# Performance work log

Hardware: AMD Instinct MI355X
Metric: run time of the kernel (lower is better)

## Reference

```python
import jax, jax.numpy as jnp
import numpy as np
import math

N = 100000
E = 800000
H = 256
TDIM = 32
NTYPES = 22
NLAYERS = 2


def layer_norm(x, g, b, eps=1e-5):
    mu = jnp.mean(x, axis=-1, keepdims=True)
    var = jnp.var(x, axis=-1, keepdims=True)
    return (x - mu) * jax.lax.rsqrt(var + eps) * g + b


def setup_inputs() -> dict:
    key = jax.random.key(0)
    ks = jax.random.split(key, 16)
    s = 1.0 / math.sqrt(H)
    inp = {
        "clause_reprs": jax.random.normal(ks[0], (N, H), dtype=jnp.float32),
        "timestamps": jax.random.uniform(ks[1], (N,), dtype=jnp.float32) * 10000.0,
        "deriv_types": jax.random.randint(ks[2], (N,), 0, NTYPES),
        "derivation_edges": jax.random.randint(ks[3], (2, E), 0, N),
        # params
        "emb_table": jax.random.normal(ks[4], (NTYPES, H), dtype=jnp.float32),
        "temp_W": jax.random.normal(ks[5], (TDIM, H), dtype=jnp.float32) / math.sqrt(TDIM),
        "temp_b": jnp.zeros((H,), jnp.float32),
        "fus_W1": jax.random.normal(ks[6], (3 * H, H), dtype=jnp.float32) / math.sqrt(3 * H),
        "fus_b1": jnp.zeros((H,), jnp.float32),
        "fus_W2": jax.random.normal(ks[7], (H, H), dtype=jnp.float32) * s,
        "fus_b2": jnp.zeros((H,), jnp.float32),
        "in_g": jnp.ones((H,), jnp.float32),
        "in_b": jnp.zeros((H,), jnp.float32),
        "deriv_W": jax.random.normal(ks[8], (NLAYERS, 2 * H, H), dtype=jnp.float32) / math.sqrt(2 * H),
        "deriv_b": jnp.zeros((NLAYERS, H), jnp.float32),
        "dn_g": jnp.ones((NLAYERS, H), jnp.float32),
        "dn_b": jnp.zeros((NLAYERS, H), jnp.float32),
    }
    return inp


def reference(clause_reprs, timestamps, deriv_types, derivation_edges,
              emb_table, temp_W, temp_b, fus_W1, fus_b1, fus_W2, fus_b2,
              in_g, in_b, deriv_W, deriv_b, dn_g, dn_b):
    # --- temporal sinusoidal encoding -> projection ---
    half = TDIM // 2
    freqs = jnp.exp(-math.log(10000.0) * jnp.arange(half, dtype=jnp.float32) / half)
    angles = timestamps[:, None] * freqs[None, :]                      # (N, half)
    pe = jnp.concatenate([jnp.sin(angles), jnp.cos(angles)], axis=-1)  # (N, TDIM)
    temporal_enc = pe @ temp_W + temp_b                                # (N, H)
    # --- derivation type embedding ---
    deriv_enc = emb_table[deriv_types]                                 # (N, H)
    # --- input fusion + residual + LN ---
    cat = jnp.concatenate([clause_reprs, temporal_enc, deriv_enc], axis=-1)
    fused = jax.nn.relu(cat @ fus_W1 + fus_b1) @ fus_W2 + fus_b2
    x = layer_norm(fused + clause_reprs, in_g, in_b)
    # --- derivation message passing along DAG edges (parent -> child) ---
    src, dst = derivation_edges[0], derivation_edges[1]
    count = jnp.zeros((N, 1), jnp.float32).at[dst].add(1.0)
    count = jnp.maximum(count, 1.0)
    for l in range(NLAYERS):
        parent_msgs = x[src]                                           # (E, H) gather
        agg = jnp.zeros_like(x).at[dst].add(parent_msgs) / count       # (N, H) scatter-add
        combined = jnp.concatenate([x, agg], axis=-1)                  # (N, 2H)
        update = jax.nn.relu(combined @ deriv_W[l] + deriv_b[l])
        x = layer_norm(x + update, dn_g[l], dn_b[l])
    return x
```

## Files before the change

### kernel.cpp

```cpp
#include <hip/hip_runtime.h>
#include <hip/hip_bf16.h>
#include <math.h>

#define N_NODES 100000
#define N_EDGES 800000
#define H 256
#define NTYPES 22
#define SCAN_G 98
#define GRID_G ((N_NODES + 63) / 64)

typedef __attribute__((ext_vector_type(8))) short short8;
typedef __attribute__((ext_vector_type(4))) float f32x4;
typedef unsigned short u16;

__device__ __forceinline__ u16 f2bf(float f) {
    unsigned u = __float_as_uint(f);
    u += 0x7FFF + ((u >> 16) & 1);
    return (u16)(u >> 16);
}
__device__ __forceinline__ float bf2f(u16 u) {
    return __uint_as_float(((unsigned)u) << 16);
}

__device__ __forceinline__ void gload16(const void* g, void* l) {
    __builtin_amdgcn_global_load_lds(
        (const __attribute__((address_space(1))) unsigned int*)g,
        (__attribute__((address_space(3))) unsigned int*)l, 16, 0, 0);
}

__global__ __launch_bounds__(256) void prep_small(
    const float* __restrict__ temp_W, const float* __restrict__ temp_b,
    const float* __restrict__ emb, const float* __restrict__ fus_W1,
    const float* __restrict__ fus_b1,
    float* __restrict__ C1, float* __restrict__ C2, float* __restrict__ beff)
{
    int b = blockIdx.x;
    int j = threadIdx.x;
    if (b < 32) {
        float acc = 0.f;
        #pragma unroll 8
        for (int m = 0; m < H; ++m)
            acc += temp_W[b * H + m] * fus_W1[(size_t)(H + m) * H + j];
        C1[b * H + j] = acc;
    } else if (b < 32 + NTYPES) {
        int e = b - 32;
        float acc = 0.f;
        #pragma unroll 8
        for (int m = 0; m < H; ++m)
            acc += emb[e * H + m] * fus_W1[(size_t)(2 * H + m) * H + j];
        C2[e * H + j] = acc;
    } else {
        float acc = fus_b1[j];
        #pragma unroll 8
        for (int m = 0; m < H; ++m)
            acc += temp_b[m] * fus_W1[(size_t)(H + m) * H + j];
        beff[j] = acc;
    }
}

__global__ __launch_bounds__(256) void prep_frag(
    const float* __restrict__ fus_W1, const float* __restrict__ C1,
    const float* __restrict__ fus_W2, const float* __restrict__ deriv_W,
    u16* __restrict__ wblob)
{
    int s = blockIdx.x;
    const float* src; int kbase;
    if (s < 8)       { src = fus_W1;              kbase = s * 32; }
    else if (s == 8) { src = C1;                  kbase = 0; }
    else if (s < 17) { src = fus_W2;              kbase = (s - 9) * 32; }
    else if (s < 33) { src = deriv_W;             kbase = (s - 17) * 32; }
    else             { src = deriv_W + 512 * H;   kbase = (s - 33) * 32; }
    #pragma unroll
    for (int it = 0; it < 4; ++it) {
        int c = it * 256 + threadIdx.x;
        int l = c & 63, nt = c >> 6;
        int n = (nt << 4) | (l & 15);
        int k0 = kbase + ((l >> 4) << 3);
        short8 v;
        #pragma unroll
        for (int i = 0; i < 8; ++i)
            v[i] = (short)f2bf(src[(size_t)(k0 + i) * H + n]);
        *reinterpret_cast<short8*>(wblob + (size_t)s * 8192 + (size_t)c * 8) = v;
    }
}

__global__ void count_kernel(const int* __restrict__ dst, int* __restrict__ cnt)
{
    int e = blockIdx.x * blockDim.x + threadIdx.x;
    if (e < N_EDGES) atomicAdd(&cnt[dst[e]], 1);
}

__global__ __launch_bounds__(1024) void scan1_kernel(
    const int* __restrict__ cnt, int* __restrict__ off, int* __restrict__ bsum)
{
    __shared__ int s[1024];
    int i = blockIdx.x * 1024 + threadIdx.x;
    int v = (i < N_NODES) ? cnt[i] : 0;
    s[threadIdx.x] = v;
    __syncthreads();
    #pragma unroll
    for (int o = 1; o < 1024; o <<= 1) {
        int t = (threadIdx.x >= o) ? s[threadIdx.x - o] : 0;
        __syncthreads();
        s[threadIdx.x] += t;
        __syncthreads();
    }
    if (i < N_NODES) off[i] = s[threadIdx.x];
    if (threadIdx.x == 1023) bsum[blockIdx.x] = s[1023];
}

__global__ void scan2_kernel(const int* __restrict__ bsum, int* __restrict__ bbase)
{
    if (threadIdx.x == 0) {
        int acc = 0;
        for (int b = 0; b < SCAN_G; ++b) { bbase[b] = acc; acc += bsum[b]; }
    }
}

__global__ __launch_bounds__(1024) void scan3_kernel(
    int* __restrict__ off, const int* __restrict__ bbase,
    const int* __restrict__ cnt, int* __restrict__ cursor)
{
    int i = blockIdx.x * 1024 + threadIdx.x;
    if (i < N_NODES) {
        int incl = off[i] + bbase[blockIdx.x];
        off[i] = incl;
        cursor[i] = incl - cnt[i];
    }
}

__global__ void fill_kernel(const int* __restrict__ src, const int* __restrict__ dst,
                            int* __restrict__ cursor, int* __restrict__ csr)
{
    int e = blockIdx.x * blockDim.x + threadIdx.x;
    if (e < N_EDGES) {
        int pos = atomicAdd(&cursor[dst[e]], 1);
        csr[pos] = src[e];
    }
}

__global__ __launch_bounds__(256) void gather_kernel(
    const u16* __restrict__ xb, const int* __restrict__ csr,
    const int* __restrict__ off, const int* __restrict__ cnt,
    u16* __restrict__ agg)
{
    int node = blockIdx.x * 4 + (threadIdx.x >> 6);
    int l = threadIdx.x & 63;
    int deg = cnt[node];
    int start = off[node] - deg;
    float a0 = 0.f, a1 = 0.f, a2 = 0.f, a3 = 0.f;
    float b0 = 0.f, b1 = 0.f, b2 = 0.f, b3 = 0.f;
    int j = 0;
    for (; j + 1 < deg; j += 2) {
        int s0 = csr[start + j], s1 = csr[start + j + 1];
        ushort4 v0 = *reinterpret_cast<const ushort4*>(xb + (size_t)s0 * H + l * 4);
        ushort4 v1 = *reinterpret_cast<const ushort4*>(xb + (size_t)s1 * H + l * 4);
        a0 += bf2f(v0.x); a1 += bf2f(v0.y); a2 += bf2f(v0.z); a3 += bf2f(v0.w);
        b0 += bf2f(v1.x); b1 += bf2f(v1.y); b2 += bf2f(v1.z); b3 += bf2f(v1.w);
    }
    if (j < deg) {
        int s0 = csr[start + j];
        ushort4 v0 = *reinterpret_cast<const ushort4*>(xb + (size_t)s0 * H + l * 4);
        a0 += bf2f(v0.x); a1 += bf2f(v0.y); a2 += bf2f(v0.z); a3 += bf2f(v0.w);
    }
    float sc = 1.0f / fmaxf((float)deg, 1.0f);
    ushort4 o;
    o.x = f2bf((a0 + b0) * sc); o.y = f2bf((a1 + b1) * sc);
    o.z = f2bf((a2 + b2) * sc); o.w = f2bf((a3 + b3) * sc);
    *reinterpret_cast<ushort4*>(agg + (size_t)node * H + l * 4) = o;
}

__device__ __forceinline__ void mfma_step(const u16* Af, const u16* Bf,
                                          int w, int l, f32x4 acc[4][4])
{
    short8 a[4];
    #pragma unroll
    for (int m = 0; m < 4; ++m)
        a[m] = *reinterpret_cast<const short8*>(Af + (size_t)((m << 6) | l) * 8);
    #pragma unroll
    for (int n = 0; n < 4; ++n) {
        short8 b = *reinterpret_cast<const short8*>(
            Bf + (size_t)((((w << 2) | n) << 6) | l) * 8);
        #pragma unroll
        for (int m = 0; m < 4; ++m)
            acc[m][n] = __builtin_amdgcn_mfma_f32_16x16x32_bf16(a[m], b, acc[m][n],
                                                                0, 0, 0);
    }
}

__global__ __launch_bounds__(256, 3) void k12_mfma(
    const float* __restrict__ clause, const float* __restrict__ ts,
    const int* __restrict__ types, const u16* __restrict__ wblob,
    const float* __restrict__ C2, const float* __restrict__ beff,
    const float* __restrict__ b2, const float* __restrict__ gW,
    const float* __restrict__ bW, u16* __restrict__ xb)
{
    __shared__ __align__(16) u16 Af[2048];
    __shared__ __align__(16) u16 Bf[8192];
    __shared__ __align__(16) u16 hs[16384];
    int tid = threadIdx.x, w = tid >> 6, l = tid & 63;
    int g = l >> 4, c0 = l & 15;
    int i0 = blockIdx.x * 64;
    int rowA = min(i0 + ((w << 4) | c0), N_NODES - 1);
    int kcol = g << 3;
    f32x4 acc[4][4] = {};

    for (int t = 0; t < 9; ++t) {
        if (t < 8) {
            const float* p = clause + (size_t)rowA * H + t * 32 + kcol;
            float4 a = *reinterpret_cast<const float4*>(p);
            float4 b = *reinterpret_cast<const float4*>(p + 4);
            short8 v;
            v[0] = (short)f2bf(a.x); v[1] = (short)f2bf(a.y);
            v[2] = (short)f2bf(a.z); v[3] = (short)f2bf(a.w);
            v[4] = (short)f2bf(b.x); v[5] = (short)f2bf(b.y);
            v[6] = (short)f2bf(b.z); v[7] = (short)f2bf(b.w);
            *reinterpret_cast<short8*>(Af + (size_t)((w << 6) | l) * 8) = v;
        } else {
            float tsv = ts[rowA];
            short8 v;
            #pragma unroll
            for (int i = 0; i < 8; ++i) {
                int k = kcol + i;
                float fr = expf(-0.57564627324851f * (float)(k & 15));
                float ang = tsv * fr;
                float pv = (k < 16) ? sinf(ang) : cosf(ang);
                v[i] = (short)f2bf(pv);
            }
            *reinterpret_cast<short8*>(Af + (size_t)((w << 6) | l) * 8) = v;
        }
        #pragma unroll
        for (int it = 0; it < 4; ++it) {
            int c = (it << 8) + tid;
            gload16(wblob + (size_t)t * 8192 + (size_t)c * 8, Bf + (size_t)c * 8);
        }
        __syncthreads();
        mfma_step(Af, Bf, w, l, acc);
        __syncthreads();
    }

    {
        float bev[4];
        #pragma unroll
        for (int n = 0; n < 4; ++n) bev[n] = beff[(w << 6) | (n << 4) | c0];
        #pragma unroll
        for (int m = 0; m < 4; ++m) {
            #pragma unroll
            for (int r = 0; r < 4; ++r) {
                int rl = (m << 4) + (g << 2) + r;
                int tp = types[min(i0 + rl, N_NODES - 1)];
                const float* c2r = C2 + (size_t)tp * H;
                #pragma unroll
                for (int n = 0; n < 4; ++n) {
                    int col = (w << 6) | (n << 4) | c0;
                    float val = fmaxf(acc[m][n][r] + bev[n] + c2r[col], 0.f);
                    hs[((rl << 8) + col) ^ ((rl & 7) << 3)] = f2bf(val);
                }
            }
        }
    }
    __syncthreads();

    #pragma unroll
    for (int m = 0; m < 4; ++m)
        #pragma unroll
        for (int n = 0; n < 4; ++n)
            acc[m][n] = (f32x4){0.f, 0.f, 0.f, 0.f};

    for (int t = 0; t < 8; ++t) {
        #pragma unroll
        for (int it = 0; it < 4; ++it) {
            int c = (it << 8) + tid;
            gload16(wblob + (size_t)(9 + t) * 8192 + (size_t)c * 8,
                    Bf + (size_t)c * 8);
        }
        __syncthreads();
        short8 a[4];
        int colb = (t << 5) + kcol;
        #pragma unroll
        for (int m = 0; m < 4; ++m) {
            int rl2 = (m << 4) | c0;
            a[m] = *reinterpret_cast<const short8*>(
                &hs[((rl2 << 8) + colb) ^ ((c0 & 7) << 3)]);
        }
        #pragma unroll
        for (int n = 0; n < 4; ++n) {
            short8 b = *reinterpret_cast<const short8*>(
                Bf + (size_t)((((w << 2) | n) << 6) | l) * 8);
            #pragma unroll
            for (int m = 0; m < 4; ++m)
                acc[m][n] = __builtin_amdgcn_mfma_f32_16x16x32_bf16(a[m], b,
                                                                    acc[m][n], 0, 0, 0);
        }
        __syncthreads();
    }

    float2* red = reinterpret_cast<float2*>(Af);
    float bv[4], gv[4], bbv[4];
    #pragma unroll
    for (int n = 0; n < 4; ++n) {
        int col = (w << 6) | (n << 4) | c0;
        bv[n] = b2[col]; gv[n] = gW[col]; bbv[n] = bW[col];
    }
    #pragma unroll
    for (int m = 0; m < 4; ++m) {
        #pragma unroll
        for (int r = 0; r < 4; ++r) {
            int rl = (m << 4) + (g << 2) + r;
            int rowc = min(i0 + rl, N_NODES - 1);
            const float* cr = clause + (size_t)rowc * H;
            float s = 0.f, q = 0.f;
            #pragma unroll
            for (int n = 0; n < 4; ++n) {
                float pv = acc[m][n][r] + bv[n] + cr[(w << 6) | (n << 4) | c0];
                acc[m][n][r] = pv;
                s += pv; q += pv * pv;
            }
            #pragma unroll
            for (int o = 1; o < 16; o <<= 1) {
                s += __shfl_xor(s, o);
                q += __shfl_xor(q, o);
            }
            if (c0 == 0) red[(rl << 2) | w] = make_float2(s, q);
        }
    }
    __syncthreads();
    #pragma unroll
    for (int m = 0; m < 4; ++m) {
        #pragma unroll
        for (int r = 0; r < 4; ++r) {
            int rl = (m << 4) + (g << 2) + r;
            int row = i0 + rl;
            float2 t0 = red[(rl << 2) | 0], t1 = red[(rl << 2) | 1];
            float2 t2 = red[(rl << 2) | 2], t3 = red[(rl << 2) | 3];
            float S = t0.x + t1.x + t2.x + t3.x;
            float Q = t0.y + t1.y + t2.y + t3.y;
            float mu = S * (1.0f / 256.0f);
            float rstd = rsqrtf(Q * (1.0f / 256.0f) - mu * mu + 1e-5f);
            if (row < N_NODES) {
                #pragma unroll
                for (int n = 0; n < 4; ++n) {
                    int col = (w << 6) | (n << 4) | c0;
                    float val = (acc[m][n][r] - mu) * rstd * gv[n] + bbv[n];
                    xb[(size_t)row * H + col] = f2bf(val);
                }
            }
        }
    }
}

template<bool FINAL>
__global__ __launch_bounds__(256, 4) void k5_mfma(
    const u16* __restrict__ xb, const u16* __restrict__ aggb,
    const u16* __restrict__ wblob, const float* __restrict__ bl,
    const float* __restrict__ gl, const float* __restrict__ bnl,
    u16* __restrict__ xbout, float* __restrict__ xout)
{
    __shared__ __align__(16) u16 Af[4096];
    __shared__ __align__(16) u16 Bf[16384];
    int tid = threadIdx.x, w = tid >> 6, l = tid & 63;
    int g = l >> 4, c0 = l & 15;
    int i0 = blockIdx.x * 64;
    int rowA = min(i0 + ((w << 4) | c0), N_NODES - 1);
    int kcol = g << 3;
    f32x4 acc[4][4] = {};

    for (int t = 0; t < 8; ++t) {
        const u16* sb = (t < 4) ? xb : aggb;
        const u16* ap = sb + (size_t)rowA * H + ((t & 3) << 6) + kcol;
        gload16(ap,      Af + (size_t)((w << 6) | l) * 8);
        gload16(ap + 32, Af + 2048 + (size_t)((w << 6) | l) * 8);
        const u16* wk = wblob + (size_t)(t << 1) * 8192;
        #pragma unroll
        for (int it = 0; it < 4; ++it) {
            int c = (it << 8) + tid;
            gload16(wk + (size_t)c * 8,        Bf + (size_t)c * 8);
            gload16(wk + 8192 + (size_t)c * 8, Bf + 8192 + (size_t)c * 8);
        }
        __syncthreads();
        mfma_step(Af, Bf, w, l, acc);
        mfma_step(Af + 2048, Bf + 8192, w, l, acc);
        __syncthreads();
    }

    float2* red = reinterpret_cast<float2*>(Af);
    float bv[4], gv[4], bbv[4];
    #pragma unroll
    for (int n = 0; n < 4; ++n) {
        int col = (w << 6) | (n << 4) | c0;
        bv[n] = bl[col]; gv[n] = gl[col]; bbv[n] = bnl[col];
    }
    #pragma unroll
    for (int m = 0; m < 4; ++m) {
        #pragma unroll
        for (int r = 0; r < 4; ++r) {
            int rl = (m << 4) + (g << 2) + r;
            int rowc = min(i0 + rl, N_NODES - 1);
            const u16* xr = xb + (size_t)rowc * H;
            float s = 0.f, q = 0.f;
            #pragma unroll
            for (int n = 0; n < 4; ++n) {
                int col = (w << 6) | (n << 4) | c0;
                float pv = bf2f(xr[col]) + fmaxf(acc[m][n][r] + bv[n], 0.f);
                acc[m][n][r] = pv;
                s += pv; q += pv * pv;
            }
            #pragma unroll
            for (int o = 1; o < 16; o <<= 1) {
                s += __shfl_xor(s, o);
                q += __shfl_xor(q, o);
            }
            if (c0 == 0) red[(rl << 2) | w] = make_float2(s, q);
        }
    }
    __syncthreads();
    #pragma unroll
    for (int m = 0; m < 4; ++m) {
        #pragma unroll
        for (int r = 0; r < 4; ++r) {
            int rl = (m << 4) + (g << 2) + r;
            int row = i0 + rl;
            float2 t0 = red[(rl << 2) | 0], t1 = red[(rl << 2) | 1];
            float2 t2 = red[(rl << 2) | 2], t3 = red[(rl << 2) | 3];
            float S = t0.x + t1.x + t2.x + t3.x;
            float Q = t0.y + t1.y + t2.y + t3.y;
            float mu = S * (1.0f / 256.0f);
            float rstd = rsqrtf(Q * (1.0f / 256.0f) - mu * mu + 1e-5f);
            if (row < N_NODES) {
                #pragma unroll
                for (int n = 0; n < 4; ++n) {
                    int col = (w << 6) | (n << 4) | c0;
                    float val = (acc[m][n][r] - mu) * rstd * gv[n] + bbv[n];
                    if (FINAL) xout[(size_t)row * H + col] = val;
                    else       xbout[(size_t)row * H + col] = f2bf(val);
                }
            }
        }
    }
}

extern "C" void kernel_launch(void* const* d_in, const int* in_sizes, int n_in,
                              void* d_out, int out_size, void* d_ws, size_t ws_size,
                              hipStream_t stream)
{
    const float* clause  = (const float*)d_in[0];
    const float* ts      = (const float*)d_in[1];
    const int*   types   = (const int*)  d_in[2];
    const int*   edges   = (const int*)  d_in[3];
    const float* emb     = (const float*)d_in[4];
    const float* temp_W  = (const float*)d_in[5];
    const float* temp_b  = (const float*)d_in[6];
    const float* fus_W1  = (const float*)d_in[7];
    const float* fus_b1  = (const float*)d_in[8];
    const float* fus_W2  = (const float*)d_in[9];
    const float* fus_b2  = (const float*)d_in[10];
    const float* in_g    = (const float*)d_in[11];
    const float* in_b    = (const float*)d_in[12];
    const float* deriv_W = (const float*)d_in[13];
    const float* deriv_b = (const float*)d_in[14];
    const float* dn_g    = (const float*)d_in[15];
    const float* dn_b    = (const float*)d_in[16];

    char* p = (char*)d_ws;
    float* C1   = (float*)p;            p += 32 * H * 4;
    float* C2   = (float*)p;            p += NTYPES * H * 4;
    float* beff = (float*)p;            p += H * 4;
    int* cnt    = (int*)p;              p += N_NODES * 4;
    int* off    = (int*)p;              p += N_NODES * 4;
    int* cursor = (int*)p;              p += N_NODES * 4;
    int* bsum   = (int*)p;              p += 128 * 4;
    int* bbase  = (int*)p;              p += 128 * 4;
    int* csr    = (int*)p;              p += N_EDGES * 4;
    u16* wblob  = (u16*)p;              p += 49 * 8192 * 2;
    u16* xb16   = (u16*)p;              p += (size_t)N_NODES * H * 2;
    u16* aggb16 = (u16*)p;              p += (size_t)N_NODES * H * 2;
    float* x    = (float*)d_out;

    const int* src = edges;
    const int* dst = edges + N_EDGES;

    prep_small<<<32 + NTYPES + 1, 256, 0, stream>>>(temp_W, temp_b, emb, fus_W1,
                                                    fus_b1, C1, C2, beff);
    prep_frag<<<49, 256, 0, stream>>>(fus_W1, C1, fus_W2, deriv_W, wblob);

    hipMemsetAsync(cnt, 0, N_NODES * sizeof(int), stream);
    count_kernel<<<(N_EDGES + 255) / 256, 256, 0, stream>>>(dst, cnt);
    scan1_kernel<<<SCAN_G, 1024, 0, stream>>>(cnt, off, bsum);
    scan2_kernel<<<1, 64, 0, stream>>>(bsum, bbase);
    scan3_kernel<<<SCAN_G, 1024, 0, stream>>>(off, bbase, cnt, cursor);
    fill_kernel<<<(N_EDGES + 255) / 256, 256, 0, stream>>>(src, dst, cursor, csr);

    k12_mfma<<<GRID_G, 256, 0, stream>>>(clause, ts, types, wblob, C2, beff,
                                         fus_b2, in_g, in_b, xb16);

    gather_kernel<<<N_NODES / 4, 256, 0, stream>>>(xb16, csr, off, cnt, aggb16);
    k5_mfma<false><<<GRID_G, 256, 0, stream>>>(
        xb16, aggb16, wblob + (size_t)17 * 8192,
        deriv_b, dn_g, dn_b, xb16, nullptr);
    gather_kernel<<<N_NODES / 4, 256, 0, stream>>>(xb16, csr, off, cnt, aggb16);
    k5_mfma<true><<<GRID_G, 256, 0, stream>>>(
        xb16, aggb16, wblob + (size_t)33 * 8192,
        deriv_b + H, dn_g + H, dn_b + H, nullptr, x);
}
```

Before: 564.6 us.

## Split fused MLP kernel, use 128-row 512-thread MFMA tiles, pre-convert clause to bf16

The clause input is converted to bf16 once up front. The fused first-stage kernel is split into two MFMA kernels, k1 and k2, with the ReLU hidden activations written to global memory in bf16. All GEMM kernels now use 128-row tiles with 8 waves in a 2x4 arrangement, which doubles weight reuse per block. The weight rows are permuted (pi2) so each lane can write four consecutive output columns as one vectorized ushort4 store. This adds an extra round trip through global memory for the hidden layer and an extra conversion pass, in exchange for less LDS per block and better weight reuse.

```diff
diff --git a/kernel.cpp b/kernel.cpp
--- a/kernel.cpp
+++ b/kernel.cpp
@@ -7,7 +7,7 @@
 #define H 256
 #define NTYPES 22
 #define SCAN_G 98
-#define GRID_G ((N_NODES + 63) / 64)
+#define GRID5 ((N_NODES + 127) / 128)
 
 typedef __attribute__((ext_vector_type(8))) short short8;
 typedef __attribute__((ext_vector_type(4))) float f32x4;
@@ -21,11 +21,28 @@
 __device__ __forceinline__ float bf2f(u16 u) {
     return __uint_as_float(((unsigned)u) << 16);
 }
+__device__ __forceinline__ int pi2(int k) {
+    return (k & 192) | ((k & 3) << 4) | ((k >> 2) & 15);
+}
 
 __device__ __forceinline__ void gload16(const void* g, void* l) {
     __builtin_amdgcn_global_load_lds(
         (const __attribute__((address_space(1))) unsigned int*)g,
         (__attribute__((address_space(3))) unsigned int*)l, 16, 0, 0);
+}
+
+__global__ __launch_bounds__(256) void conv_bf16(
+    const float* __restrict__ src, u16* __restrict__ dst)
+{
+    size_t i = (size_t)blockIdx.x * 256 + threadIdx.x;
+    const float4 a = ((const float4*)src)[i * 2];
+    const float4 b = ((const float4*)src)[i * 2 + 1];
+    short8 v;
+    v[0] = (short)f2bf(a.x); v[1] = (short)f2bf(a.y);
+    v[2] = (short)f2bf(a.z); v[3] = (short)f2bf(a.w);
+    v[4] = (short)f2bf(b.x); v[5] = (short)f2bf(b.y);
+    v[6] = (short)f2bf(b.z); v[7] = (short)f2bf(b.w);
+    ((short8*)dst)[i] = v;
 }
 
 __global__ __launch_bounds__(256) void prep_small(
@@ -64,22 +81,32 @@
     u16* __restrict__ wblob)
 {
     int s = blockIdx.x;
-    const float* src; int kbase;
-    if (s < 8)       { src = fus_W1;              kbase = s * 32; }
-    else if (s == 8) { src = C1;                  kbase = 0; }
-    else if (s < 17) { src = fus_W2;              kbase = (s - 9) * 32; }
-    else if (s < 33) { src = deriv_W;             kbase = (s - 17) * 32; }
-    else             { src = deriv_W + 512 * H;   kbase = (s - 33) * 32; }
     #pragma unroll
     for (int it = 0; it < 4; ++it) {
         int c = it * 256 + threadIdx.x;
         int l = c & 63, nt = c >> 6;
-        int n = (nt << 4) | (l & 15);
-        int k0 = kbase + ((l >> 4) << 3);
+        int ncol = (nt << 4) | (l & 15);
+        int kin = (l >> 4) << 3;
         short8 v;
         #pragma unroll
-        for (int i = 0; i < 8; ++i)
-            v[i] = (short)f2bf(src[(size_t)(k0 + i) * H + n]);
+        for (int i = 0; i < 8; ++i) {
+            const float* srcp;
+            if (s < 8) {
+                srcp = fus_W1 + (size_t)(s * 32 + kin + i) * H;
+            } else if (s == 8) {
+                srcp = C1 + (size_t)(kin + i) * H;
+            } else if (s < 17) {
+                int k = (s - 9) * 32 + kin + i;
+                srcp = fus_W2 + (size_t)pi2(k) * H;
+            } else if (s < 33) {
+                int k = (s - 17) * 32 + kin + i;
+                srcp = deriv_W + (size_t)((k >> 8) * 256 + pi2(k & 255)) * H;
+            } else {
+                int k = (s - 33) * 32 + kin + i;
+                srcp = deriv_W + (size_t)(512 + (k >> 8) * 256 + pi2(k & 255)) * H;
+            }
+            v[i] = (short)f2bf(srcp[ncol]);
+        }
         *reinterpret_cast<short8*>(wblob + (size_t)s * 8192 + (size_t)c * 8) = v;
     }
 }
@@ -170,149 +197,139 @@
     *reinterpret_cast<ushort4*>(agg + (size_t)node * H + l * 4) = o;
 }
 
-__device__ __forceinline__ void mfma_step(const u16* Af, const u16* Bf,
-                                          int w, int l, f32x4 acc[4][4])
-{
-    short8 a[4];
+__device__ __forceinline__ void stageA8(u16* Af, const u16* __restrict__ src,
+                                        int i0, int kbase, int tid)
+{
+    int rt = tid >> 6, l = tid & 63;
+    int row = min(i0 + rt * 16 + (l & 15), N_NODES - 1);
+    gload16(src + (size_t)row * H + kbase + ((l >> 4) << 3), Af + (tid << 3));
+}
+
+__device__ __forceinline__ void stageB8(u16* Bf, const u16* __restrict__ wk, int tid)
+{
+    gload16(wk + ((size_t)tid << 3),         Bf + (tid << 3));
+    gload16(wk + ((size_t)(tid + 512) << 3), Bf + ((tid + 512) << 3));
+}
+
+__device__ __forceinline__ void mfma_step8(const u16* Af, const u16* Bf,
+                                           int wm, int wn, int l, f32x4 acc[4][4])
+{
+    short8 a[4], b[4];
     #pragma unroll
     for (int m = 0; m < 4; ++m)
-        a[m] = *reinterpret_cast<const short8*>(Af + (size_t)((m << 6) | l) * 8);
-    #pragma unroll
-    for (int n = 0; n < 4; ++n) {
-        short8 b = *reinterpret_cast<const short8*>(
-            Bf + (size_t)((((w << 2) | n) << 6) | l) * 8);
+        a[m] = *reinterpret_cast<const short8*>(Af + ((((wm << 2) | m) << 6 | l) << 3));
+    #pragma unroll
+    for (int n = 0; n < 4; ++n)
+        b[n] = *reinterpret_cast<const short8*>(Bf + ((((wn << 2) | n) << 6 | l) << 3));
+    #pragma unroll
+    for (int n = 0; n < 4; ++n)
         #pragma unroll
         for (int m = 0; m < 4; ++m)
-            acc[m][n] = __builtin_amdgcn_mfma_f32_16x16x32_bf16(a[m], b, acc[m][n],
-                                                                0, 0, 0);
-    }
-}
-
-__global__ __launch_bounds__(256, 3) void k12_mfma(
-    const float* __restrict__ clause, const float* __restrict__ ts,
+            acc[m][n] = __builtin_amdgcn_mfma_f32_16x16x32_bf16(a[m], b[n],
+                                                                acc[m][n], 0, 0, 0);
+}
+
+__global__ __launch_bounds__(512, 4) void k1_mfma(
+    const u16* __restrict__ cb, const float* __restrict__ ts,
     const int* __restrict__ types, const u16* __restrict__ wblob,
     const float* __restrict__ C2, const float* __restrict__ beff,
-    const float* __restrict__ b2, const float* __restrict__ gW,
-    const float* __restrict__ bW, u16* __restrict__ xb)
-{
-    __shared__ __align__(16) u16 Af[2048];
+    u16* __restrict__ hb)
+{
+    __shared__ __align__(16) u16 Af[4096];
     __shared__ __align__(16) u16 Bf[8192];
-    __shared__ __align__(16) u16 hs[16384];
     int tid = threadIdx.x, w = tid >> 6, l = tid & 63;
-    int g = l >> 4, c0 = l & 15;
-    int i0 = blockIdx.x * 64;
-    int rowA = min(i0 + ((w << 4) | c0), N_NODES - 1);
-    int kcol = g << 3;
+    int wm = w >> 2, wn = w & 3, g = l >> 4, c0 = l & 15;
+    int i0 = blockIdx.x * 128;
     f32x4 acc[4][4] = {};
 
     for (int t = 0; t < 9; ++t) {
         if (t < 8) {
-            const float* p = clause + (size_t)rowA * H + t * 32 + kcol;
-            float4 a = *reinterpret_cast<const float4*>(p);
-            float4 b = *reinterpret_cast<const float4*>(p + 4);
-            short8 v;
-            v[0] = (short)f2bf(a.x); v[1] = (short)f2bf(a.y);
-            v[2] = (short)f2bf(a.z); v[3] = (short)f2bf(a.w);
-            v[4] = (short)f2bf(b.x); v[5] = (short)f2bf(b.y);
-            v[6] = (short)f2bf(b.z); v[7] = (short)f2bf(b.w);
-            *reinterpret_cast<short8*>(Af + (size_t)((w << 6) | l) * 8) = v;
+            stageA8(Af, cb, i0, t * 32, tid);
         } else {
-            float tsv = ts[rowA];
+            int rt = tid >> 6;
+            int row = min(i0 + rt * 16 + c0, N_NODES - 1);
+            float tsv = ts[row];
             short8 v;
             #pragma unroll
             for (int i = 0; i < 8; ++i) {
-                int k = kcol + i;
+                int k = (g << 3) + i;
                 float fr = expf(-0.57564627324851f * (float)(k & 15));
                 float ang = tsv * fr;
                 float pv = (k < 16) ? sinf(ang) : cosf(ang);
                 v[i] = (short)f2bf(pv);
             }
-            *reinterpret_cast<short8*>(Af + (size_t)((w << 6) | l) * 8) = v;
-        }
-        #pragma unroll
-        for (int it = 0; it < 4; ++it) {
-            int c = (it << 8) + tid;
-            gload16(wblob + (size_t)t * 8192 + (size_t)c * 8, Bf + (size_t)c * 8);
-        }
-        __syncthreads();
-        mfma_step(Af, Bf, w, l, acc);
-        __syncthreads();
-    }
-
-    {
-        float bev[4];
-        #pragma unroll
-        for (int n = 0; n < 4; ++n) bev[n] = beff[(w << 6) | (n << 4) | c0];
-        #pragma unroll
-        for (int m = 0; m < 4; ++m) {
-            #pragma unroll
-            for (int r = 0; r < 4; ++r) {
-                int rl = (m << 4) + (g << 2) + r;
-                int tp = types[min(i0 + rl, N_NODES - 1)];
-                const float* c2r = C2 + (size_t)tp * H;
-                #pragma unroll
-                for (int n = 0; n < 4; ++n) {
-                    int col = (w << 6) | (n << 4) | c0;
-                    float val = fmaxf(acc[m][n][r] + bev[n] + c2r[col], 0.f);
-                    hs[((rl << 8) + col) ^ ((rl & 7) << 3)] = f2bf(val);
-                }
-            }
-        }
-    }
-    __syncthreads();
-
-    #pragma unroll
-    for (int m = 0; m < 4; ++m)
-        #pragma unroll
-        for (int n = 0; n < 4; ++n)
-            acc[m][n] = (f32x4){0.f, 0.f, 0.f, 0.f};
+            *reinterpret_cast<short8*>(Af + (tid << 3)) = v;
+        }
+        stageB8(Bf, wblob + (size_t)t * 8192, tid);
+        __syncthreads();
+        mfma_step8(Af, Bf, wm, wn, l, acc);
+        __syncthreads();
+    }
+
+    float bev[4];
+    #pragma unroll
+    for (int n = 0; n < 4; ++n) bev[n] = beff[(((wn << 2) | n) << 4) | c0];
+    #pragma unroll
+    for (int m = 0; m < 4; ++m) {
+        #pragma unroll
+        for (int r = 0; r < 4; ++r) {
+            int rl = (((wm << 2) | m) << 4) + (g << 2) + r;
+            int row = i0 + rl;
+            bool ok = row < N_NODES;
+            int tp = types[ok ? row : 0];
+            const float* c2r = C2 + (size_t)tp * H;
+            ushort4 o;
+            float v0 = fmaxf(acc[m][0][r] + bev[0] + c2r[((wn << 2) << 4) | c0], 0.f);
+            float v1 = fmaxf(acc[m][1][r] + bev[1] + c2r[(((wn << 2) | 1) << 4) | c0], 0.f);
+            float v2 = fmaxf(acc[m][2][r] + bev[2] + c2r[(((wn << 2) | 2) << 4) | c0], 0.f);
+            float v3 = fmaxf(acc[m][3][r] + bev[3] + c2r[(((wn << 2) | 3) << 4) | c0], 0.f);
+            o.x = f2bf(v0); o.y = f2bf(v1); o.z = f2bf(v2); o.w = f2bf(v3);
+            if (ok)
+                *reinterpret_cast<ushort4*>(hb + (size_t)row * H + (wn << 6) + (c0 << 2)) = o;
+        }
+    }
+}
+
+__global__ __launch_bounds__(512, 4) void k2_mfma(
+    const u16* __restrict__ hb, const u16* __restrict__ cb,
+    const u16* __restrict__ wblob, const float* __restrict__ b2,
+    const float* __restrict__ gW, const float* __restrict__ bW,
+    u16* __restrict__ xb)
+{
+    __shared__ __align__(16) u16 Af[4096];
+    __shared__ __align__(16) u16 Bf[8192];
+    int tid = threadIdx.x, w = tid >> 6, l = tid & 63;
+    int wm = w >> 2, wn = w & 3, g = l >> 4, c0 = l & 15;
+    int i0 = blockIdx.x * 128;
+    f32x4 acc[4][4] = {};
 
     for (int t = 0; t < 8; ++t) {
-        #pragma unroll
-        for (int it = 0; it < 4; ++it) {
-            int c = (it << 8) + tid;
-            gload16(wblob + (size_t)(9 + t) * 8192 + (size_t)c * 8,
-                    Bf + (size_t)c * 8);
-        }
-        __syncthreads();
-        short8 a[4];
-        int colb = (t << 5) + kcol;
-        #pragma unroll
-        for (int m = 0; m < 4; ++m) {
-            int rl2 = (m << 4) | c0;
-            a[m] = *reinterpret_cast<const short8*>(
-                &hs[((rl2 << 8) + colb) ^ ((c0 & 7) << 3)]);
-        }
-        #pragma unroll
-        for (int n = 0; n < 4; ++n) {
-            short8 b = *reinterpret_cast<const short8*>(
-                Bf + (size_t)((((w << 2) | n) << 6) | l) * 8);
-            #pragma unroll
-            for (int m = 0; m < 4; ++m)
-                acc[m][n] = __builtin_amdgcn_mfma_f32_16x16x32_bf16(a[m], b,
-                                                                    acc[m][n], 0, 0, 0);
-        }
-        __syncthreads();
-    }
-
+        stageA8(Af, hb, i0, t * 32, tid);
+        stageB8(Bf, wblob + (size_t)t * 8192, tid);
+        __syncthreads();
+        mfma_step8(Af, Bf, wm, wn, l, acc);
+        __syncthreads();
+    }
+
+    float bv[4], gv[4], bbv[4];
+    int lc[4];
+    #pragma unroll
+    for (int n = 0; n < 4; ++n) {
+        lc[n] = (((wn << 2) | n) << 4) | c0;
+        bv[n] = b2[lc[n]]; gv[n] = gW[lc[n]]; bbv[n] = bW[lc[n]];
+    }
     float2* red = reinterpret_cast<float2*>(Af);
-    float bv[4], gv[4], bbv[4];
-    #pragma unroll
-    for (int n = 0; n < 4; ++n) {
-        int col = (w << 6) | (n << 4) | c0;
-        bv[n] = b2[col]; gv[n] = gW[col]; bbv[n] = bW[col];
-    }
     #pragma unroll
     for (int m = 0; m < 4; ++m) {
         #pragma unroll
         for (int r = 0; r < 4; ++r) {
-            int rl = (m << 4) + (g << 2) + r;
+            int rl = (((wm << 2) | m) << 4) + (g << 2) + r;
             int rowc = min(i0 + rl, N_NODES - 1);
-            const float* cr = clause + (size_t)rowc * H;
+            const u16* cr = cb + (size_t)rowc * H;
             float s = 0.f, q = 0.f;
             #pragma unroll
             for (int n = 0; n < 4; ++n) {
-                float pv = acc[m][n][r] + bv[n] + cr[(w << 6) | (n << 4) | c0];
+                float pv = acc[m][n][r] + bv[n] + bf2f(cr[lc[n]]);
                 acc[m][n][r] = pv;
                 s += pv; q += pv * pv;
             }
@@ -321,7 +338,7 @@
                 s += __shfl_xor(s, o);
                 q += __shfl_xor(q, o);
             }
-            if (c0 == 0) red[(rl << 2) | w] = make_float2(s, q);
+            if (c0 == 0) red[(rl << 2) | wn] = make_float2(s, q);
         }
     }
     __syncthreads();
@@ -329,7 +346,7 @@
     for (int m = 0; m < 4; ++m) {
         #pragma unroll
         for (int r = 0; r < 4; ++r) {
-            int rl = (m << 4) + (g << 2) + r;
+            int rl = (((wm << 2) | m) << 4) + (g << 2) + r;
             int row = i0 + rl;
             float2 t0 = red[(rl << 2) | 0], t1 = red[(rl << 2) | 1];
             float2 t2 = red[(rl << 2) | 2], t3 = red[(rl << 2) | 3];
@@ -338,79 +355,70 @@
             float mu = S * (1.0f / 256.0f);
             float rstd = rsqrtf(Q * (1.0f / 256.0f) - mu * mu + 1e-5f);
             if (row < N_NODES) {
-                #pragma unroll
-                for (int n = 0; n < 4; ++n) {
-                    int col = (w << 6) | (n << 4) | c0;
-                    float val = (acc[m][n][r] - mu) * rstd * gv[n] + bbv[n];
-                    xb[(size_t)row * H + col] = f2bf(val);
-                }
+                ushort4 o;
+                o.x = f2bf((acc[m][0][r] - mu) * rstd * gv[0] + bbv[0]);
+                o.y = f2bf((acc[m][1][r] - mu) * rstd * gv[1] + bbv[1]);
+                o.z = f2bf((acc[m][2][r] - mu) * rstd * gv[2] + bbv[2]);
+                o.w = f2bf((acc[m][3][r] - mu) * rstd * gv[3] + bbv[3]);
+                *reinterpret_cast<ushort4*>(xb + (size_t)row * H + (wn << 6) + (c0 << 2)) = o;
             }
         }
     }
 }
 
 template<bool FINAL>
-__global__ __launch_bounds__(256, 4) void k5_mfma(
+__global__ __launch_bounds__(512, 4) void k5_mfma(
     const u16* __restrict__ xb, const u16* __restrict__ aggb,
     const u16* __restrict__ wblob, const float* __restrict__ bl,
     const float* __restrict__ gl, const float* __restrict__ bnl,
     u16* __restrict__ xbout, float* __restrict__ xout)
 {
     __shared__ __align__(16) u16 Af[4096];
-    __shared__ __align__(16) u16 Bf[16384];
+    __shared__ __align__(16) u16 Bf[8192];
     int tid = threadIdx.x, w = tid >> 6, l = tid & 63;
-    int g = l >> 4, c0 = l & 15;
-    int i0 = blockIdx.x * 64;
-    int rowA = min(i0 + ((w << 4) | c0), N_NODES - 1);
-    int kcol = g << 3;
+    int wm = w >> 2, wn = w & 3, g = l >> 4, c0 = l & 15;
+    int i0 = blockIdx.x * 128;
     f32x4 acc[4][4] = {};
 
-    for (int t = 0; t < 8; ++t) {
-        const u16* sb = (t < 4) ? xb : aggb;
-        const u16* ap = sb + (size_t)rowA * H + ((t & 3) << 6) + kcol;
-        gload16(ap,      Af + (size_t)((w << 6) | l) * 8);
-        gload16(ap + 32, Af + 2048 + (size_t)((w << 6) | l) * 8);
-        const u16* wk = wblob + (size_t)(t << 1) * 8192;
-        #pragma unroll
-        for (int it = 0; it < 4; ++it) {
-            int c = (it << 8) + tid;
-            gload16(wk + (size_t)c * 8,        Bf + (size_t)c * 8);
-            gload16(wk + 8192 + (size_t)c * 8, Bf + 8192 + (size_t)c * 8);
-        }
-        __syncthreads();
-        mfma_step(Af, Bf, w, l, acc);
-        mfma_step(Af + 2048, Bf + 8192, w, l, acc);
-        __syncthreads();
-    }
-
+    for (int t = 0; t < 16; ++t) {
+        stageA8(Af, (t < 8) ? xb : aggb, i0, (t & 7) * 32, tid);
+        stageB8(Bf, wblob + (size_t)t * 8192, tid);
+        __syncthreads();
+        mfma_step8(Af, Bf, wm, wn, l, acc);
+        __syncthreads();
+    }
+
+    float bv[4], gv[4], bbv[4];
+    int lc[4];
+    #pragma unroll
+    for (int n = 0; n < 4; ++n) {
+        lc[n] = (((wn << 2) | n) << 4) | c0;
+        bv[n] = bl[lc[n]]; gv[n] = gl[lc[n]]; bbv[n] = bnl[lc[n]];
+    }
     float2* red = reinterpret_cast<float2*>(Af);
-    float bv[4], gv[4], bbv[4];
-    #pragma unroll
-    for (int n = 0; n < 4; ++n) {
-        int col = (w << 6) | (n << 4) | c0;
-        bv[n] = bl[col]; gv[n] = gl[col]; bbv[n] = bnl[col];
-    }
     #pragma unroll
     for (int m = 0; m < 4; ++m) {
         #pragma unroll
         for (int r = 0; r < 4; ++r) {
-            int rl = (m << 4) + (g << 2) + r;
+            int rl = (((wm << 2) | m) << 4) + (g << 2) + r;
             int rowc = min(i0 + rl, N_NODES - 1);
-            const u16* xr = xb + (size_t)rowc * H;
+            ushort4 xr = *reinterpret_cast<const ushort4*>(
+                xb + (size_t)rowc * H + (wn << 6) + (c0 << 2));
             float s = 0.f, q = 0.f;
-            #pragma unroll
-            for (int n = 0; n < 4; ++n) {
-                int col = (w << 6) | (n << 4) | c0;
-                float pv = bf2f(xr[col]) + fmaxf(acc[m][n][r] + bv[n], 0.f);
-                acc[m][n][r] = pv;
-                s += pv; q += pv * pv;
-            }
+            float p0 = bf2f(xr.x) + fmaxf(acc[m][0][r] + bv[0], 0.f);
+            float p1 = bf2f(xr.y) + fmaxf(acc[m][1][r] + bv[1], 0.f);
+            float p2 = bf2f(xr.z) + fmaxf(acc[m][2][r] + bv[2], 0.f);
+            float p3 = bf2f(xr.w) + fmaxf(acc[m][3][r] + bv[3], 0.f);
+            acc[m][0][r] = p0; acc[m][1][r] = p1;
+            acc[m][2][r] = p2; acc[m][3][r] = p3;
+            s = p0 + p1 + p2 + p3;
+            q = p0 * p0 + p1 * p1 + p2 * p2 + p3 * p3;
             #pragma unroll
             for (int o = 1; o < 16; o <<= 1) {
                 s += __shfl_xor(s, o);
                 q += __shfl_xor(q, o);
             }
-            if (c0 == 0) red[(rl << 2) | w] = make_float2(s, q);
+            if (c0 == 0) red[(rl << 2) | wn] = make_float2(s, q);
         }
     }
     __syncthreads();
@@ -418,7 +426,7 @@
     for (int m = 0; m < 4; ++m) {
         #pragma unroll
         for (int r = 0; r < 4; ++r) {
-            int rl = (m << 4) + (g << 2) + r;
+            int rl = (((wm << 2) | m) << 4) + (g << 2) + r;
             int row = i0 + rl;
             float2 t0 = red[(rl << 2) | 0], t1 = red[(rl << 2) | 1];
             float2 t2 = red[(rl << 2) | 2], t3 = red[(rl << 2) | 3];
@@ -427,12 +435,19 @@
             float mu = S * (1.0f / 256.0f);
             float rstd = rsqrtf(Q * (1.0f / 256.0f) - mu * mu + 1e-5f);
             if (row < N_NODES) {
-                #pragma unroll
-                for (int n = 0; n < 4; ++n) {
-                    int col = (w << 6) | (n << 4) | c0;
-                    float val = (acc[m][n][r] - mu) * rstd * gv[n] + bbv[n];
-                    if (FINAL) xout[(size_t)row * H + col] = val;
-                    else       xbout[(size_t)row * H + col] = f2bf(val);
+                if (FINAL) {
+                    #pragma unroll
+                    for (int n = 0; n < 4; ++n)
+                        xout[(size_t)row * H + lc[n]] =
+                            (acc[m][n][r] - mu) * rstd * gv[n] + bbv[n];
+                } else {
+                    ushort4 o;
+                    o.x = f2bf((acc[m][0][r] - mu) * rstd * gv[0] + bbv[0]);
+                    o.y = f2bf((acc[m][1][r] - mu) * rstd * gv[1] + bbv[1]);
+                    o.z = f2bf((acc[m][2][r] - mu) * rstd * gv[2] + bbv[2]);
+                    o.w = f2bf((acc[m][3][r] - mu) * rstd * gv[3] + bbv[3]);
+                    *reinterpret_cast<ushort4*>(
+                        xbout + (size_t)row * H + (wn << 6) + (c0 << 2)) = o;
                 }
             }
         }
@@ -472,13 +487,14 @@
     int* bbase  = (int*)p;              p += 128 * 4;
     int* csr    = (int*)p;              p += N_EDGES * 4;
     u16* wblob  = (u16*)p;              p += 49 * 8192 * 2;
-    u16* xb16   = (u16*)p;              p += (size_t)N_NODES * H * 2;
-    u16* aggb16 = (u16*)p;              p += (size_t)N_NODES * H * 2;
+    u16* B1     = (u16*)p;              p += (size_t)N_NODES * H * 2;
+    u16* B2     = (u16*)p;              p += (size_t)N_NODES * H * 2;
     float* x    = (float*)d_out;
 
     const int* src = edges;
     const int* dst = edges + N_EDGES;
 
+    conv_bf16<<<(N_NODES * H / 8 + 255) / 256, 256, 0, stream>>>(clause, B1);
     prep_small<<<32 + NTYPES + 1, 256, 0, stream>>>(temp_W, temp_b, emb, fus_W1,
                                                     fus_b1, C1, C2, beff);
     prep_frag<<<49, 256, 0, stream>>>(fus_W1, C1, fus_W2, deriv_W, wblob);
@@ -490,15 +506,15 @@
     scan3_kernel<<<SCAN_G, 1024, 0, stream>>>(off, bbase, cnt, cursor);
     fill_kernel<<<(N_EDGES + 255) / 256, 256, 0, stream>>>(src, dst, cursor, csr);
 
-    k12_mfma<<<GRID_G, 256, 0, stream>>>(clause, ts, types, wblob, C2, beff,
-                                         fus_b2, in_g, in_b, xb16);
-
-    gather_kernel<<<N_NODES / 4, 256, 0, stream>>>(xb16, csr, off, cnt, aggb16);
-    k5_mfma<false><<<GRID_G, 256, 0, stream>>>(
-        xb16, aggb16, wblob + (size_t)17 * 8192,
-        deriv_b, dn_g, dn_b, xb16, nullptr);
-    gather_kernel<<<N_NODES / 4, 256, 0, stream>>>(xb16, csr, off, cnt, aggb16);
-    k5_mfma<true><<<GRID_G, 256, 0, stream>>>(
-        xb16, aggb16, wblob + (size_t)33 * 8192,
-        deriv_b + H, dn_g + H, dn_b + H, nullptr, x);
-}
+    k1_mfma<<<GRID5, 512, 0, stream>>>(B1, ts, types, wblob, C2, beff, B2);
+    k2_mfma<<<GRID5, 512, 0, stream>>>(B2, B1, wblob + (size_t)9 * 8192,
+                                       fus_b2, in_g, in_b, B2);
+
+    gather_kernel<<<N_NODES / 4, 256, 0, stream>>>(B2, csr, off, cnt, B1);
+    k5_mfma<false><<<GRID5, 512, 0, stream>>>(
+        B2, B1, wblob + (size_t)17 * 8192, deriv_b, dn_g, dn_b, B2, nullptr);
+    gather_kernel<<<N_NODES / 4, 256, 0, stream>>>(B2, csr, off, cnt, B1);
+    k5_mfma<true><<<GRID5, 512, 0, stream>>>(
+        B2, B1, wblob + (size_t)33 * 8192, deriv_b + H, dn_g + H, dn_b + H,
+        nullptr, x);
+}
```

New measurement: 527.8 us. 1.07x faster.
